# Optimization experiments

Measured on AMD Instinct MI355X. Metric: run time of the kernel, lower is better.

## Reference

```python
import jax, jax.numpy as jnp
import numpy as np
from jax import lax

V_PATCH_NUMS = (1, 2, 3, 4, 5, 6, 8, 10, 13, 16)
SHARE_K = 4
RESI = 0.5  # abs(quant_resi)


def _area_matrix(pn, H):
    # F.interpolate(mode='area') == adaptive_avg_pool2d: uniform mean over [floor, ceil) window
    W = np.zeros((pn, H), np.float32)
    for i in range(pn):
        s = int(np.floor(i * H / pn)); e = int(np.ceil((i + 1) * H / pn))
        W[i, s:e] = 1.0 / (e - s)
    return W


def _cubic(x, a=-0.75):
    x = abs(x)
    if x <= 1.0:
        return (a + 2) * x**3 - (a + 3) * x**2 + 1
    if x < 2.0:
        return a * x**3 - 5 * a * x**2 + 8 * a * x - 4 * a
    return 0.0


def _bicubic_matrix(out, inp):
    # torch bicubic, align_corners=False, a=-0.75, border-clamped (separable 1D matrix)
    W = np.zeros((out, inp), np.float32)
    for i in range(out):
        src = (i + 0.5) * inp / out - 0.5
        i0 = int(np.floor(src)); t = src - i0
        for k in range(-1, 3):
            j = min(max(i0 + k, 0), inp - 1)
            W[i, j] += _cubic(k - t)
    return W


def _phi_select(si, SN, K=SHARE_K):
    ticks = np.linspace(1 / 3 / K, 1 - 1 / 3 / K, K) if K == 4 else np.linspace(1 / 2 / K, 1 - 1 / 2 / K, K)
    return int(np.argmin(np.abs(ticks - si / (SN - 1))))


def _phi(h, w, b):
    # Phi: h*(1-r) + conv3x3(h)*r
    y = lax.conv_general_dilated(h, w, (1, 1), 'SAME',
                                 dimension_numbers=('NCHW', 'OIHW', 'NCHW'))
    y = y + b[None, :, None, None]
    return h * (1.0 - RESI) + y * RESI


def reference(f, embedding, phi_w, phi_b):
    # Multi-scale residual vector quantization (VectorQuantizer2 hot path).
    # f: [B, C, 16, 16] latent; embedding: [V, C]; phi_w: [K, C, C, 3, 3]; phi_b: [K, C]
    B, C, H, Wd = f.shape
    SN = len(V_PATCH_NUMS)
    e2 = jnp.sum(embedding**2, axis=1)  # [V]
    f_hat = jnp.zeros_like(f)
    f_rest = f
    for si, pn in enumerate(V_PATCH_NUMS):
        if si != SN - 1:
            A = jnp.asarray(_area_matrix(pn, H))
            z = jnp.einsum('ph,bchw,qw->bcpq', A, f_rest, A)  # area downsample to pn x pn
        else:
            z = f_rest
        zf = z.transpose(0, 2, 3, 1).reshape(-1, C)  # [B*pn*pn, C]
        # squared-distance cdist + argmin codebook lookup
        d = jnp.sum(zf**2, axis=1, keepdims=True) - 2.0 * (zf @ embedding.T) + e2[None, :]
        idx = jnp.argmin(d, axis=1)  # [B*pn*pn]
        h = embedding[idx].reshape(B, pn, pn, C).transpose(0, 3, 1, 2)  # gather -> [B,C,pn,pn]
        if si != SN - 1:
            U = jnp.asarray(_bicubic_matrix(H, pn))
            h = jnp.einsum('hp,bcpq,wq->bchw', U, h, U)  # bicubic upsample to H x W
        k = _phi_select(si, SN)
        h = _phi(h, phi_w[k], phi_b[k])  # partially-shared Phi residual refinement
        f_hat = f_hat + h
        f_rest = f_rest - h
    return f_hat


def setup_inputs() -> dict:
    key = jax.random.key(0)
    k1, k2, k3 = jax.random.split(key, 3)
    f = jax.random.normal(k1, (64, 32, 16, 16), dtype=jnp.float32)
    embedding = jax.random.normal(k2, (4096, 32), dtype=jnp.float32)
    phi_w = jax.random.normal(k3, (4, 32, 32, 3, 3), dtype=jnp.float32) * 0.05
    phi_b = jnp.zeros((4, 32), dtype=jnp.float32)
    return {"f": f, "embedding": embedding, "phi_w": phi_w, "phi_b": phi_b}
```

## Files before the change

kernel.cpp:

```cpp
#include <hip/hip_runtime.h>
#include <cmath>


#define BB 64
#define CC 32
#define HH 16
#define VV 4096
#define NTOT (BB*CC*HH*HH)

typedef __attribute__((ext_vector_type(8))) short bf16x8;
typedef __attribute__((ext_vector_type(4))) float f32x4;

__device__ __forceinline__ double cubicw(double x) {
    x = fabs(x);
    const double a = -0.75;
    if (x <= 1.0) return ((a + 2.0) * x - (a + 3.0)) * x * x + 1.0;
    if (x < 2.0)  return (((a * x - 5.0 * a) * x + 8.0 * a) * x - 4.0 * a);
    return 0.0;
}

__device__ __forceinline__ unsigned int ordf(float d) {
    unsigned int b = __float_as_uint(d);
    return (b & 0x80000000u) ? ~b : (b | 0x80000000u);
}

__device__ __forceinline__ short f2bf(float x) {
    unsigned u = __float_as_uint(x);
    unsigned r = (u + 0x7fffu + ((u >> 16) & 1u)) >> 16;
    return (short)r;
}
__device__ __forceinline__ float bf2f(short h) {
    return __uint_as_float(((unsigned)(unsigned short)h) << 16);
}

__global__ void init_k(const float* __restrict__ f, const float* __restrict__ E,
                       float* __restrict__ f_rest, float* __restrict__ f_hat,
                       float* __restrict__ e2, float* __restrict__ z,
                       unsigned short* __restrict__ est) {
    int i = blockIdx.x * 256 + threadIdx.x;
    if (i < NTOT) { f_rest[i] = f[i]; f_hat[i] = 0.f; }
    if (i < VV) {
        float s = 0.f;
        int tile = i >> 4, n = i & 15;
        #pragma unroll
        for (int c = 0; c < CC; ++c) {
            float x = E[i * CC + c];
            s += x * x;
            if (est) {
                short h = f2bf(x); float rm = x - bf2f(h);
                short m = f2bf(rm); float rl = rm - bf2f(m);
                short l = f2bf(rl);
                int idx = tile * 1536 + (n * 4 + (c >> 3)) * 8 + (c & 7);
                est[idx]        = (unsigned short)h;
                est[idx + 512]  = (unsigned short)m;
                est[idx + 1024] = (unsigned short)l;
            }
        }
        e2[i] = s;
    }
    if (i < BB * CC) {
        const float* src = f + (size_t)i * (HH * HH);
        float s = 0.f;
        for (int j = 0; j < HH * HH; ++j) s += src[j];
        z[i] = s * (1.0f / 256.0f);
    }
}

__global__ __launch_bounds__(256, 4) void argsmall_k(const float* __restrict__ z,
        const float* __restrict__ E, const float* __restrict__ e2,
        unsigned long long* __restrict__ bestk, int M, int G, int gsz) {
    const int t = threadIdx.x;
    int m = blockIdx.x * 64 + (t & 63);
    int w = __builtin_amdgcn_readfirstlane(t >> 6);
    int wg = blockIdx.y * 4 + w;
    int v0 = wg * gsz;
    float zr[CC]; float z2 = 0.f;
    const float4* zp = (const float4*)(z + (size_t)m * CC);
    #pragma unroll
    for (int c4 = 0; c4 < 8; ++c4) {
        float4 v = zp[c4];
        zr[c4*4+0] = v.x; zr[c4*4+1] = v.y; zr[c4*4+2] = v.z; zr[c4*4+3] = v.w;
        z2 += v.x*v.x + v.y*v.y + v.z*v.z + v.w*v.w;
    }
    const float* e = E + (size_t)v0 * CC;
    float best = 3.4e38f; int bv = v0;
    for (int v = v0; v < v0 + gsz; v += 2, e += 2 * CC) {
        float a0 = 0.f, a1 = 0.f, b0 = 0.f, b1 = 0.f;
        #pragma unroll
        for (int c = 0; c < CC; c += 2) {
            a0 = fmaf(zr[c],   e[c],      a0);
            a1 = fmaf(zr[c+1], e[c+1],    a1);
            b0 = fmaf(zr[c],   e[CC+c],   b0);
            b1 = fmaf(zr[c+1], e[CC+c+1], b1);
        }
        float dA = fmaf(-2.f, a0 + a1, z2 + e2[v]);
        float dB = fmaf(-2.f, b0 + b1, z2 + e2[v+1]);
        if (dA < best) { best = dA; bv = v; }
        if (dB < best) { best = dB; bv = v + 1; }
    }
    bestk[(size_t)m * G + wg] = ((unsigned long long)ordf(best) << 32) |
                                (unsigned long long)(unsigned int)bv;
}

__global__ __launch_bounds__(256, 4) void argmf_k(const unsigned short* __restrict__ zs,
        const unsigned short* __restrict__ est, const float* __restrict__ e2,
        unsigned long long* __restrict__ bestk, int M, int G, int gsz) {
    const int t = threadIdx.x;
    const int g = blockIdx.y;
    const int v0 = g * gsz;
    const int lane = t & 63;
    const int w = t >> 6;
    const int n = lane & 15, kq = lane >> 4;

    int tb[2]; bf16x8 ah[2], am[2], al[2];
    #pragma unroll
    for (int pt = 0; pt < 2; ++pt) {
        int tb0 = blockIdx.x * 128 + w * 32 + pt * 16;
        if (tb0 > M - 16) tb0 = M - 16;
        tb[pt] = tb0;
        const unsigned short* zp = zs + (size_t)(tb0 + n) * 96 + kq * 8;
        ah[pt] = *(const bf16x8*)(zp);
        am[pt] = *(const bf16x8*)(zp + 32);
        al[pt] = *(const bf16x8*)(zp + 64);
    }

    float bd[2][4]; int bc[2][4];
    #pragma unroll
    for (int pt = 0; pt < 2; ++pt)
        #pragma unroll
        for (int r = 0; r < 4; ++r) { bd[pt][r] = 3.4e38f; bc[pt][r] = 0; }

    const int nct = gsz >> 4;
    const unsigned short* ep = est + (size_t)(v0 >> 4) * 1536 +
                               (size_t)(n * 4 + kq) * 8;
    const float* e2p = e2 + v0 + n;
    bf16x8 eh = *(const bf16x8*)(ep);
    bf16x8 em = *(const bf16x8*)(ep + 512);
    bf16x8 el = *(const bf16x8*)(ep + 1024);
    float e2c = *e2p;
    for (int ct = 0; ct < nct; ++ct) {
        bf16x8 ceh = eh, cem = em, cel = el; float ce2 = e2c;
        if (ct + 1 < nct) {
            ep += 1536; e2p += 16;
            eh = *(const bf16x8*)(ep);
            em = *(const bf16x8*)(ep + 512);
            el = *(const bf16x8*)(ep + 1024);
            e2c = *e2p;
        }
        #pragma unroll
        for (int pt = 0; pt < 2; ++pt) {
            f32x4 Ca = {0.f, 0.f, 0.f, 0.f};
            f32x4 Cb = {ce2, ce2, ce2, ce2};
            Ca = __builtin_amdgcn_mfma_f32_16x16x32_bf16(ah[pt], ceh, Ca, 0, 0, 0);
            Cb = __builtin_amdgcn_mfma_f32_16x16x32_bf16(am[pt], ceh, Cb, 0, 0, 0);
            Ca = __builtin_amdgcn_mfma_f32_16x16x32_bf16(ah[pt], cem, Ca, 0, 0, 0);
            Cb = __builtin_amdgcn_mfma_f32_16x16x32_bf16(al[pt], ceh, Cb, 0, 0, 0);
            Ca = __builtin_amdgcn_mfma_f32_16x16x32_bf16(ah[pt], cel, Ca, 0, 0, 0);
            Cb = __builtin_amdgcn_mfma_f32_16x16x32_bf16(am[pt], cem, Cb, 0, 0, 0);
            #pragma unroll
            for (int r = 0; r < 4; ++r) {
                float d = Ca[r] + Cb[r];
                if (d < bd[pt][r]) { bd[pt][r] = d; bc[pt][r] = ct; }
            }
        }
    }
    #pragma unroll
    for (int pt = 0; pt < 2; ++pt) {
        #pragma unroll
        for (int r = 0; r < 4; ++r) {
            int v = v0 + bc[pt][r] * 16 + n;
            unsigned long long k = ((unsigned long long)ordf(bd[pt][r]) << 32) |
                                   (unsigned long long)(unsigned int)v;
            #pragma unroll
            for (int msk = 1; msk < 16; msk <<= 1) {
                unsigned long long o = __shfl_xor(k, msk);
                if (o < k) k = o;
            }
            if (n == 0)
                bestk[(size_t)(tb[pt] + kq * 4 + r) * G + g] = k;
        }
    }
}

__global__ __launch_bounds__(256, 4) void argbig_k(const float* __restrict__ z,
        const float* __restrict__ E, const float* __restrict__ e2,
        unsigned long long* __restrict__ bestk, int M, int G, int gsz) {
    __shared__ float s_e[128 * CC];
    __shared__ float s_e2[128];
    const int T = gridDim.x * 256;
    const int g = blockIdx.y;
    const int v0 = g * gsz;
    {
        const float4* src = (const float4*)(E + (size_t)v0 * CC);
        float4* dst = (float4*)s_e;
        for (int i = threadIdx.x; i < gsz * 8; i += 256) dst[i] = src[i];
        if (threadIdx.x < gsz) s_e2[threadIdx.x] = e2[v0 + threadIdx.x];
    }
    int   mm[2];
    bool  act[2];
    float zr[2][CC];
    float z2[2];
    #pragma unroll
    for (int pt = 0; pt < 2; ++pt) {
        int m0 = blockIdx.x * 256 + threadIdx.x + pt * T;
        act[pt] = (m0 < M);
        int m = act[pt] ? m0 : M - 1;
        mm[pt] = m;
        const float4* zp = (const float4*)(z + (size_t)m * CC);
        float zz = 0.f;
        #pragma unroll
        for (int c4 = 0; c4 < 8; ++c4) {
            float4 v = zp[c4];
            zr[pt][c4*4+0] = v.x; zr[pt][c4*4+1] = v.y;
            zr[pt][c4*4+2] = v.z; zr[pt][c4*4+3] = v.w;
            zz += v.x*v.x + v.y*v.y + v.z*v.z + v.w*v.w;
        }
        z2[pt] = zz;
    }
    __syncthreads();
    float best[2]; int bv[2];
    #pragma unroll
    for (int pt = 0; pt < 2; ++pt) { best[pt] = 3.4e38f; bv[pt] = v0; }
    const float4* ev = (const float4*)s_e;
    for (int vi = 0; vi < gsz; ++vi, ev += 8) {
        float4 e0 = ev[0], e1 = ev[1], e2v = ev[2], e3 = ev[3];
        float4 e4 = ev[4], e5 = ev[5], e6v = ev[6], e7 = ev[7];
        float ef[CC] = {e0.x,e0.y,e0.z,e0.w, e1.x,e1.y,e1.z,e1.w,
                        e2v.x,e2v.y,e2v.z,e2v.w, e3.x,e3.y,e3.z,e3.w,
                        e4.x,e4.y,e4.z,e4.w, e5.x,e5.y,e5.z,e5.w,
                        e6v.x,e6v.y,e6v.z,e6v.w, e7.x,e7.y,e7.z,e7.w};
        float a0 = 0.f, a1 = 0.f, b0 = 0.f, b1 = 0.f;
        #pragma unroll
        for (int c = 0; c < CC; c += 2) {
            a0 = fmaf(zr[0][c],   ef[c],   a0);
            a1 = fmaf(zr[0][c+1], ef[c+1], a1);
            b0 = fmaf(zr[1][c],   ef[c],   b0);
            b1 = fmaf(zr[1][c+1], ef[c+1], b1);
        }
        float e2c = s_e2[vi];
        float dA = fmaf(-2.f, a0 + a1, z2[0] + e2c);
        float dB = fmaf(-2.f, b0 + b1, z2[1] + e2c);
        int v = v0 + vi;
        if (dA < best[0]) { best[0] = dA; bv[0] = v; }
        if (dB < best[1]) { best[1] = dB; bv[1] = v; }
    }
    #pragma unroll
    for (int pt = 0; pt < 2; ++pt)
        if (act[pt])
            bestk[(size_t)mm[pt] * G + g] =
                ((unsigned long long)ordf(best[pt]) << 32) |
                (unsigned long long)(unsigned int)bv[pt];
}

__global__ __launch_bounds__(512) void fuse_k(const unsigned long long* __restrict__ bestk,
                      const float* __restrict__ E,
                      const float* __restrict__ pw, const float* __restrict__ pb,
                      float* __restrict__ f_hat, float* __restrict__ f_rest,
                      float* __restrict__ z_next, unsigned short* __restrict__ zsn,
                      int pn, int G, int TPP, int kphi, int pnn) {
    __shared__ float s_buf[CC * 18 * 20];
    __shared__ float s_scratch[256 * 36];
    __shared__ float s_pw[CC * 3 * 4 * 8];
    __shared__ int   s_idx[256];
    __shared__ float s_w[HH][4];
    __shared__ int   s_j[HH][4];
    __shared__ unsigned long long s_red[256];
    const int t   = threadIdx.x;
    const int cog = blockIdx.x;
    const int b   = blockIdx.y;
    const int P   = pn * pn;
    const int half = t >> 8;
    const int tl   = t & 255;

    {
        int p = t / TPP, sub = t - p * TPP;
        unsigned long long bk = ~0ull;
        if (p < P) {
            const unsigned long long* kp = bestk + (size_t)(b * P + p) * G;
            for (int gg = sub; gg < G; gg += TPP) {
                unsigned long long o = kp[gg];
                if (o < bk) bk = o;
            }
        }
        int bfly = TPP > 64 ? 64 : TPP;
        for (int msk = 1; msk < bfly; msk <<= 1) {
            unsigned long long o = __shfl_xor(bk, msk);
            if (o < bk) bk = o;
        }
        if (p < P) {
            if (TPP <= 64) {
                if (sub == 0) s_red[p] = bk;
            } else {
                int K = TPP >> 6;
                if ((sub & 63) == 0) s_red[p * K + (sub >> 6)] = bk;
            }
        }
    }
    if (t < HH) {
        double src = (t + 0.5) * (double)pn / 16.0 - 0.5;
        double fi = floor(src); int i0 = (int)fi; double tt = src - fi;
        #pragma unroll
        for (int k = 0; k < 4; ++k) {
            int j = i0 - 1 + k; j = j < 0 ? 0 : (j > pn - 1 ? pn - 1 : j);
            s_j[t][k] = j;
            s_w[t][k] = (float)cubicw((double)(k - 1) - tt);
        }
    }
    {
        const float* src = pw + ((size_t)(kphi * CC + cog * 8)) * CC * 9;
        for (int i = t; i < 8 * CC * 9; i += 512) {
            int l  = i / (CC * 9);
            int r  = i - l * (CC * 9);
            int ci = r / 9; int kk = r - ci * 9;
            int kh = kk / 3; int kw = kk - kh * 3;
            int cp = l >> 1, ce = l & 1;
            s_pw[ci * 96 + kh * 32 + cp * 8 + ce * 4 + kw] = src[i];
        }
    }
    __syncthreads();
    if (t < P) {
        unsigned long long r = s_red[(TPP <= 64) ? t : t * (TPP >> 6)];
        if (TPP > 64) {
            int K = TPP >> 6;
            for (int j2 = 1; j2 < K; ++j2) {
                unsigned long long o = s_red[t * K + j2];
                if (o < r) r = o;
            }
        }
        s_idx[t] = (int)(unsigned int)(r & 0xffffffffull);
    }
    __syncthreads();

    if (tl < HH * pn) {
        int h = tl / pn, q = tl % pn;
        int cbase = half * 16;
        float acc[16];
        #pragma unroll
        for (int c = 0; c < 16; ++c) acc[c] = 0.f;
        #pragma unroll
        for (int k = 0; k < 4; ++k) {
            float wv = s_w[h][k];
            if (wv == 0.0f) continue;
            int row = s_idx[s_j[h][k] * pn + q];
            const float4* er = (const float4*)(E + (size_t)row * CC + cbase);
            #pragma unroll
            for (int c4 = 0; c4 < 4; ++c4) {
                float4 e4 = er[c4];
                acc[c4*4+0] = fmaf(wv, e4.x, acc[c4*4+0]);
                acc[c4*4+1] = fmaf(wv, e4.y, acc[c4*4+1]);
                acc[c4*4+2] = fmaf(wv, e4.z, acc[c4*4+2]);
                acc[c4*4+3] = fmaf(wv, e4.w, acc[c4*4+3]);
            }
        }
        float* dst = &s_scratch[(h * pn + q) * 36 + cbase];
        *(float4*)(dst + 0)  = make_float4(acc[0],  acc[1],  acc[2],  acc[3]);
        *(float4*)(dst + 4)  = make_float4(acc[4],  acc[5],  acc[6],  acc[7]);
        *(float4*)(dst + 8)  = make_float4(acc[8],  acc[9],  acc[10], acc[11]);
        *(float4*)(dst + 12) = make_float4(acc[12], acc[13], acc[14], acc[15]);
    }
    __syncthreads();

    {
        int h = tl >> 4, w = tl & 15;
        int cbase = half * 16;
        float acc[16];
        #pragma unroll
        for (int c = 0; c < 16; ++c) acc[c] = 0.f;
        #pragma unroll
        for (int k = 0; k < 4; ++k) {
            float wh = s_w[w][k];
            int j = s_j[w][k];
            const float4* sp4 = (const float4*)&s_scratch[(h * pn + j) * 36 + cbase];
            float4 v0 = sp4[0], v1 = sp4[1], v2 = sp4[2], v3 = sp4[3];
            acc[0]  = fmaf(wh, v0.x, acc[0]);  acc[1]  = fmaf(wh, v0.y, acc[1]);
            acc[2]  = fmaf(wh, v0.z, acc[2]);  acc[3]  = fmaf(wh, v0.w, acc[3]);
            acc[4]  = fmaf(wh, v1.x, acc[4]);  acc[5]  = fmaf(wh, v1.y, acc[5]);
            acc[6]  = fmaf(wh, v1.z, acc[6]);  acc[7]  = fmaf(wh, v1.w, acc[7]);
            acc[8]  = fmaf(wh, v2.x, acc[8]);  acc[9]  = fmaf(wh, v2.y, acc[9]);
            acc[10] = fmaf(wh, v2.z, acc[10]); acc[11] = fmaf(wh, v2.w, acc[11]);
            acc[12] = fmaf(wh, v3.x, acc[12]); acc[13] = fmaf(wh, v3.y, acc[13]);
            acc[14] = fmaf(wh, v3.z, acc[14]); acc[15] = fmaf(wh, v3.w, acc[15]);
        }
        #pragma unroll
        for (int c = 0; c < 16; ++c)
            s_buf[((cbase + c) * 18 + h + 1) * 20 + w + 1] = acc[c];
        if (w == 0) {
            #pragma unroll
            for (int c = 0; c < 16; ++c) s_buf[((cbase + c) * 18 + h + 1) * 20] = 0.f;
        }
        if (w >= 13) {
            #pragma unroll
            for (int c = 0; c < 16; ++c) s_buf[((cbase + c) * 18 + h + 1) * 20 + w + 4] = 0.f;
        }
        if (h == 0) {
            #pragma unroll
            for (int c = 0; c < 16; ++c) {
                s_buf[((cbase + c) * 18) * 20 + w] = 0.f;
                if (w < 4) s_buf[((cbase + c) * 18) * 20 + 16 + w] = 0.f;
            }
        }
        if (h == 15) {
            #pragma unroll
            for (int c = 0; c < 16; ++c) {
                s_buf[((cbase + c) * 18 + 17) * 20 + w] = 0.f;
                if (w < 4) s_buf[((cbase + c) * 18 + 17) * 20 + 16 + w] = 0.f;
            }
        }
    }
    __syncthreads();

    const int cp  = tl >> 6;
    const int q   = (tl >> 5) & 1;
    const int s   = tl & 31;
    const int h   = s >> 1;
    const int w0  = (s & 1) * 8;
    const int wid = half * 2 + q;
    const int pos = cp * 32 + s;
    float accE[8], accO[8];
    #pragma unroll
    for (int o = 0; o < 8; ++o) { accE[o] = 0.f; accO[o] = 0.f; }
    const int ci0 = wid * 8;
    for (int ci = ci0; ci < ci0 + 8; ++ci) {
        const float* wrow = &s_pw[ci * 96 + cp * 8];
        #pragma unroll
        for (int kk = 0; kk < 3; ++kk) {
            int kh = kk + q; kh = (kh >= 3) ? kh - 3 : kh;
            const float4* xr = (const float4*)&s_buf[(ci * 18 + h + kh) * 20 + w0];
            float4 a0 = xr[0], a1 = xr[1], a2 = xr[2];
            float xf[12] = {a0.x, a0.y, a0.z, a0.w, a1.x, a1.y, a1.z, a1.w,
                            a2.x, a2.y, a2.z, a2.w};
            const float4* wp = (const float4*)(wrow + kh * 32);
            float4 wA = wp[0];
            float4 wB = wp[1];
            #pragma unroll
            for (int o = 0; o < 8; ++o) {
                accE[o] += xf[o] * wA.x + xf[o+1] * wA.y + xf[o+2] * wA.z;
                accO[o] += xf[o] * wB.x + xf[o+1] * wB.y + xf[o+2] * wB.z;
            }
        }
    }
    if (wid != 0) {
        float* dst = &s_scratch[((wid - 1) * 128 + pos) * 20];
        *(float4*)(dst +  0) = make_float4(accE[0], accE[1], accE[2], accE[3]);
        *(float4*)(dst +  4) = make_float4(accE[4], accE[5], accE[6], accE[7]);
        *(float4*)(dst +  8) = make_float4(accO[0], accO[1], accO[2], accO[3]);
        *(float4*)(dst + 12) = make_float4(accO[4], accO[5], accO[6], accO[7]);
    }
    __syncthreads();

    float4 rE0, rE1, rO0, rO1;
    if (wid == 0) {
        #pragma unroll
        for (int g2 = 0; g2 < 3; ++g2) {
            const float* sp = &s_scratch[(g2 * 128 + pos) * 20];
            float4 p0 = *(const float4*)(sp + 0), p1 = *(const float4*)(sp + 4);
            float4 p2 = *(const float4*)(sp + 8), p3 = *(const float4*)(sp + 12);
            accE[0] += p0.x; accE[1] += p0.y; accE[2] += p0.z; accE[3] += p0.w;
            accE[4] += p1.x; accE[5] += p1.y; accE[6] += p1.z; accE[7] += p1.w;
            accO[0] += p2.x; accO[1] += p2.y; accO[2] += p2.z; accO[3] += p2.w;
            accO[4] += p3.x; accO[5] += p3.y; accO[6] += p3.z; accO[7] += p3.w;
        }
        float biasE = pb[kphi * CC + cog * 8 + cp * 2];
        float biasO = pb[kphi * CC + cog * 8 + cp * 2 + 1];
        #pragma unroll
        for (int o = 0; o < 8; ++o) { accE[o] += biasE; accO[o] += biasO; }
        #pragma unroll
        for (int c = 0; c < 2; ++c) {
            const float* acc = c ? accO : accE;
            int co = cog * 8 + cp * 2 + c;
            float hf[8];
            #pragma unroll
            for (int o = 0; o < 8; ++o) {
                float hv = s_buf[(co * 18 + h + 1) * 20 + w0 + o + 1];
                hf[o] = 0.5f * hv + 0.5f * acc[o];
            }
            size_t base = ((size_t)(b * CC + co) * HH + h) * HH + w0;
            float4* fh = (float4*)(f_hat + base);
            float4* fr = (float4*)(f_rest + base);
            float4 v0 = fh[0], v1 = fh[1];
            v0.x += hf[0]; v0.y += hf[1]; v0.z += hf[2]; v0.w += hf[3];
            v1.x += hf[4]; v1.y += hf[5]; v1.z += hf[6]; v1.w += hf[7];
            fh[0] = v0; fh[1] = v1;
            float4 r0 = fr[0], r1 = fr[1];
            r0.x -= hf[0]; r0.y -= hf[1]; r0.z -= hf[2]; r0.w -= hf[3];
            r1.x -= hf[4]; r1.y -= hf[5]; r1.z -= hf[6]; r1.w -= hf[7];
            fr[0] = r0; fr[1] = r1;
            if (c) { rO0 = r0; rO1 = r1; } else { rE0 = r0; rE1 = r1; }
        }
    }

    if (pnn > 0) {
        __syncthreads();
        float* fn = s_buf;
        if (wid == 0) {
            #pragma unroll
            for (int c = 0; c < 2; ++c) {
                int cl = cp * 2 + c;
                float* d = &fn[(cl * HH + h) * HH + w0];
                float4 r0 = c ? rO0 : rE0, r1 = c ? rO1 : rE1;
                d[0] = r0.x; d[1] = r0.y; d[2] = r0.z; d[3] = r0.w;
                d[4] = r1.x; d[5] = r1.y; d[6] = r1.z; d[7] = r1.w;
            }
        }
        __syncthreads();
        int P2 = pnn * pnn;
        for (int i = t; i < P2 * 8; i += 512) {
            int cl = i & 7, pq = i >> 3;
            int q2 = pq % pnn, p2 = pq / pnn;
            int sp = (p2 * HH) / pnn, ep = ((p2 + 1) * HH + pnn - 1) / pnn;
            int sq = (q2 * HH) / pnn, eq = ((q2 + 1) * HH + pnn - 1) / pnn;
            float wgt = 1.0f / ((float)(ep - sp) * (float)(eq - sq));
            float sum = 0.f;
            for (int h2 = sp; h2 < ep; ++h2)
                for (int w2 = sq; w2 < eq; ++w2)
                    sum += fn[(cl * HH + h2) * HH + w2];
            float v = sum * wgt;
            int c = cog * 8 + cl;
            if (zsn) {
                float tv = -2.0f * v;
                size_t baz = (size_t)(b * P2 + pq) * 96 + c;
                unsigned short hh = (unsigned short)f2bf(tv);
                float rm = tv - bf2f((short)hh);
                unsigned short mm2 = (unsigned short)f2bf(rm);
                float rl = rm - bf2f((short)mm2);
                unsigned short ll = (unsigned short)f2bf(rl);
                zsn[baz] = hh; zsn[baz + 32] = mm2; zsn[baz + 64] = ll;
            } else {
                z_next[((size_t)(b * P2 + pq)) * CC + c] = v;
            }
        }
    }
}

extern "C" void kernel_launch(void* const* d_in, const int* in_sizes, int n_in,
                              void* d_out, int out_size, void* d_ws, size_t ws_size,
                              hipStream_t stream) {
    const float* f  = (const float*)d_in[0];
    const float* E  = (const float*)d_in[1];
    const float* pw = (const float*)d_in[2];
    const float* pb = (const float*)d_in[3];
    float* out = (float*)d_out;

    const size_t need_base = (size_t)(NTOT + VV) * 4 + (size_t)524288 * 8 +
                             (size_t)524288 * 4;
    const size_t need_mf = need_base + (size_t)VV * 96 * 2 +
                           (size_t)16384 * 96 * 2;
    const bool use_mf = (ws_size >= need_mf);

    float* wsf    = (float*)d_ws;
    float* f_rest = wsf;
    float* e2     = wsf + (size_t)NTOT;
    unsigned long long* bestk = (unsigned long long*)(e2 + VV);
    float* z      = (float*)(bestk + 524288);
    unsigned short* est = use_mf ? (unsigned short*)(z + 524288) : (unsigned short*)0;
    unsigned short* zs  = use_mf ? (est + (size_t)VV * 96) : (unsigned short*)0;

    int phik[10];
    {
        double start = 1.0 / 3.0 / 4.0;
        double stop  = 1.0 - 1.0 / 3.0 / 4.0;
        double step  = (stop - start) / 3.0;
        double ticks[4];
        for (int i = 0; i < 4; ++i) ticks[i] = (double)i * step + start;
        ticks[3] = stop;
        for (int si = 0; si < 10; ++si) {
            double s = (double)si / 9.0;
            int bk = 0; double bd = fabs(ticks[0] - s);
            for (int tq = 1; tq < 4; ++tq) {
                double d2 = fabs(ticks[tq] - s);
                if (d2 < bd) { bd = d2; bk = tq; }
            }
            phik[si] = bk;
        }
    }

    static const int pns[10]  = {1, 2, 3, 4, 5, 6, 8, 10, 13, 16};
    static const int grpS[10] = {256, 128, 64, 32, 32, 16, 0, 0, 0, 0};
    static const int grpF[10] = {0, 0, 0, 0, 0, 0, 128, 64, 32, 32};
    static const int grpM[10] = {0, 0, 0, 32, 32, 32, 16, 16, 8, 8};

    init_k<<<(NTOT + 255) / 256, 256, 0, stream>>>(f, E, f_rest, out, e2, z, est);

    for (int si = 0; si < 10; ++si) {
        int pn = pns[si];
        int P = pn * pn;
        int M = BB * P;
        int G, TPP;
        bool small_path = use_mf ? (pn <= 3) : (pn <= 6);
        if (small_path) {
            int grp = grpS[si];
            G = grp * 4;
            int gsz = VV / G;
            argsmall_k<<<dim3(P, grp), 256, 0, stream>>>(z, E, e2, bestk, M, G, gsz);
        } else if (use_mf) {
            G = grpM[si];
            int gsz = VV / G;
            int bx = (M + 127) / 128;
            argmf_k<<<dim3(bx, G), 256, 0, stream>>>(zs, est, e2, bestk, M, G, gsz);
        } else {
            G = grpF[si];
            int gsz = VV / G;
            int bx = (M + 511) / 512;
            argbig_k<<<dim3(bx, G), 256, 0, stream>>>(z, E, e2, bestk, M, G, gsz);
        }
        TPP = 1;
        while (TPP * 2 * P <= 512) TPP *= 2;
        int pnn = (si < 9) ? pns[si + 1] : 0;
        unsigned short* zsn = (pnn >= 4 && use_mf) ? zs : (unsigned short*)0;
        fuse_k<<<dim3(4, BB), 512, 0, stream>>>(bestk, E, pw, pb,
                                                out, f_rest, z, zsn,
                                                pn, G, TPP, phik[si], pnn);
    }
}
```

Before: 374.5 us.

## Reduce codebook argmin with atomicMin and derive f_hat from f minus f_rest

```diff
diff --git a/kernel.cpp b/kernel.cpp
--- a/kernel.cpp
+++ b/kernel.cpp
@@ -7,6 +7,8 @@
 #define HH 16
 #define VV 4096
 #define NTOT (BB*CC*HH*HH)
+#define ABASE 163840
+#define ATOT  42624
 
 typedef __attribute__((ext_vector_type(8))) short bf16x8;
 typedef __attribute__((ext_vector_type(4))) float f32x4;
@@ -34,11 +36,13 @@
 }
 
 __global__ void init_k(const float* __restrict__ f, const float* __restrict__ E,
-                       float* __restrict__ f_rest, float* __restrict__ f_hat,
+                       float* __restrict__ f_rest,
                        float* __restrict__ e2, float* __restrict__ z,
-                       unsigned short* __restrict__ est) {
+                       unsigned short* __restrict__ est,
+                       unsigned long long* __restrict__ bka) {
     int i = blockIdx.x * 256 + threadIdx.x;
-    if (i < NTOT) { f_rest[i] = f[i]; f_hat[i] = 0.f; }
+    if (i < NTOT) f_rest[i] = f[i];
+    if (bka && i < ATOT) bka[i] = ~0ull;
     if (i < VV) {
         float s = 0.f;
         int tile = i >> 4, n = i & 15;
@@ -104,7 +108,7 @@
 
 __global__ __launch_bounds__(256, 4) void argmf_k(const unsigned short* __restrict__ zs,
         const unsigned short* __restrict__ est, const float* __restrict__ e2,
-        unsigned long long* __restrict__ bestk, int M, int G, int gsz) {
+        unsigned long long* __restrict__ bka, int M, int G, int gsz) {
     const int t = threadIdx.x;
     const int g = blockIdx.y;
     const int v0 = g * gsz;
@@ -177,7 +181,7 @@
                 if (o < k) k = o;
             }
             if (n == 0)
-                bestk[(size_t)(tb[pt] + kq * 4 + r) * G + g] = k;
+                atomicMin(&bka[(size_t)(tb[pt] + kq * 4 + r)], k);
         }
     }
 }
@@ -255,7 +259,8 @@
 __global__ __launch_bounds__(512) void fuse_k(const unsigned long long* __restrict__ bestk,
                       const float* __restrict__ E,
                       const float* __restrict__ pw, const float* __restrict__ pb,
-                      float* __restrict__ f_hat, float* __restrict__ f_rest,
+                      const float* __restrict__ fsrc, float* __restrict__ fout,
+                      float* __restrict__ f_rest,
                       float* __restrict__ z_next, unsigned short* __restrict__ zsn,
                       int pn, int G, int TPP, int kphi, int pnn) {
     __shared__ float s_buf[CC * 18 * 20];
@@ -272,7 +277,10 @@
     const int half = t >> 8;
     const int tl   = t & 255;
 
-    {
+    if (G == 0) {
+        if (t < P)
+            s_idx[t] = (int)(unsigned int)(bestk[(size_t)b * P + t] & 0xffffffffull);
+    } else {
         int p = t / TPP, sub = t - p * TPP;
         unsigned long long bk = ~0ull;
         if (p < P) {
@@ -318,7 +326,7 @@
         }
     }
     __syncthreads();
-    if (t < P) {
+    if (G != 0 && t < P) {
         unsigned long long r = s_red[(TPP <= 64) ? t : t * (TPP >> 6)];
         if (TPP > 64) {
             int K = TPP >> 6;
@@ -329,7 +337,7 @@
         }
         s_idx[t] = (int)(unsigned int)(r & 0xffffffffull);
     }
-    __syncthreads();
+    if (G != 0) __syncthreads();
 
     if (tl < HH * pn) {
         int h = tl / pn, q = tl % pn;
@@ -475,16 +483,23 @@
                 hf[o] = 0.5f * hv + 0.5f * acc[o];
             }
             size_t base = ((size_t)(b * CC + co) * HH + h) * HH + w0;
-            float4* fh = (float4*)(f_hat + base);
             float4* fr = (float4*)(f_rest + base);
-            float4 v0 = fh[0], v1 = fh[1];
-            v0.x += hf[0]; v0.y += hf[1]; v0.z += hf[2]; v0.w += hf[3];
-            v1.x += hf[4]; v1.y += hf[5]; v1.z += hf[6]; v1.w += hf[7];
-            fh[0] = v0; fh[1] = v1;
             float4 r0 = fr[0], r1 = fr[1];
             r0.x -= hf[0]; r0.y -= hf[1]; r0.z -= hf[2]; r0.w -= hf[3];
             r1.x -= hf[4]; r1.y -= hf[5]; r1.z -= hf[6]; r1.w -= hf[7];
-            fr[0] = r0; fr[1] = r1;
+            if (pnn > 0) {
+                fr[0] = r0; fr[1] = r1;
+            } else {
+                const float4* fs = (const float4*)(fsrc + base);
+                float4 s0 = fs[0], s1 = fs[1];
+                float4 o0, o1;
+                o0.x = s0.x - r0.x; o0.y = s0.y - r0.y;
+                o0.z = s0.z - r0.z; o0.w = s0.w - r0.w;
+                o1.x = s1.x - r1.x; o1.y = s1.y - r1.y;
+                o1.z = s1.z - r1.z; o1.w = s1.w - r1.w;
+                float4* fo = (float4*)(fout + base);
+                fo[0] = o0; fo[1] = o1;
+            }
             if (c) { rO0 = r0; rO1 = r1; } else { rE0 = r0; rE1 = r1; }
         }
     }
@@ -554,6 +569,7 @@
     float* z      = (float*)(bestk + 524288);
     unsigned short* est = use_mf ? (unsigned short*)(z + 524288) : (unsigned short*)0;
     unsigned short* zs  = use_mf ? (est + (size_t)VV * 96) : (unsigned short*)0;
+    unsigned long long* bka = use_mf ? (bestk + ABASE) : (unsigned long long*)0;
 
     int phik[10];
     {
@@ -578,8 +594,9 @@
     static const int grpS[10] = {256, 128, 64, 32, 32, 16, 0, 0, 0, 0};
     static const int grpF[10] = {0, 0, 0, 0, 0, 0, 128, 64, 32, 32};
     static const int grpM[10] = {0, 0, 0, 32, 32, 32, 16, 16, 8, 8};
-
-    init_k<<<(NTOT + 255) / 256, 256, 0, stream>>>(f, E, f_rest, out, e2, z, est);
+    static const int aoff[10] = {0, 0, 0, 0, 1024, 2624, 4928, 9024, 15424, 26240};
+
+    init_k<<<(NTOT + 255) / 256, 256, 0, stream>>>(f, E, f_rest, e2, z, est, bka);
 
     for (int si = 0; si < 10; ++si) {
         int pn = pns[si];
@@ -587,28 +604,34 @@
         int M = BB * P;
         int G, TPP;
         bool small_path = use_mf ? (pn <= 3) : (pn <= 6);
+        const unsigned long long* fuse_bk = bestk;
         if (small_path) {
             int grp = grpS[si];
             G = grp * 4;
             int gsz = VV / G;
             argsmall_k<<<dim3(P, grp), 256, 0, stream>>>(z, E, e2, bestk, M, G, gsz);
+            TPP = 1;
+            while (TPP * 2 * P <= 512) TPP *= 2;
         } else if (use_mf) {
-            G = grpM[si];
-            int gsz = VV / G;
+            int grp = grpM[si];
+            int gsz = VV / grp;
             int bx = (M + 127) / 128;
-            argmf_k<<<dim3(bx, G), 256, 0, stream>>>(zs, est, e2, bestk, M, G, gsz);
+            unsigned long long* slice = bka + aoff[si];
+            argmf_k<<<dim3(bx, grp), 256, 0, stream>>>(zs, est, e2, slice, M, grp, gsz);
+            fuse_bk = slice;
+            G = 0; TPP = 1;
         } else {
             G = grpF[si];
             int gsz = VV / G;
             int bx = (M + 511) / 512;
             argbig_k<<<dim3(bx, G), 256, 0, stream>>>(z, E, e2, bestk, M, G, gsz);
-        }
-        TPP = 1;
-        while (TPP * 2 * P <= 512) TPP *= 2;
+            TPP = 1;
+            while (TPP * 2 * P <= 512) TPP *= 2;
+        }
         int pnn = (si < 9) ? pns[si + 1] : 0;
         unsigned short* zsn = (pnn >= 4 && use_mf) ? zs : (unsigned short*)0;
-        fuse_k<<<dim3(4, BB), 512, 0, stream>>>(bestk, E, pw, pb,
-                                                out, f_rest, z, zsn,
+        fuse_k<<<dim3(4, BB), 512, 0, stream>>>(fuse_bk, E, pw, pb,
+                                                f, out, f_rest, z, zsn,
                                                 pn, G, TPP, phik[si], pnn);
     }
 }
```

Measured after the change: 364.1 us. 1.03x faster.
